# Performance work log

Measured on AMD Instinct MI355X. Metric: run time of the kernel, lower is better.

Reference implementation:

```python
import jax, jax.numpy as jnp
import numpy as np

T = 40           # rollout steps
ATT_TEMP = 5.0   # Arbiter attention temperature
ACT_CLIP = 3.5


def setup_inputs() -> dict:
    key = jax.random.key(0)
    ks = jax.random.split(key, 6)
    B, D = 262144, 128
    # states: vel >= 0, dx > 0 (dx is a divisor)
    unscaled_s = jax.random.uniform(ks[0], (B, T, 7), dtype=jnp.float32)
    unscaled_s = unscaled_s.at[:, :, 0].set(unscaled_s[:, :, 0] * 20.0 + 5.0)   # vel
    unscaled_s = unscaled_s.at[:, :, 2].set(unscaled_s[:, :, 2] * 4.0 - 2.0)    # dv (leader)
    unscaled_s = unscaled_s.at[:, :, 3].set(unscaled_s[:, :, 3] * 50.0 + 10.0)  # dx (leader)
    unscaled_s = unscaled_s.at[:, :, 5].set(unscaled_s[:, :, 5] * 4.0 - 2.0)    # dv (merger)
    unscaled_s = unscaled_s.at[:, :, 6].set(unscaled_s[:, :, 6] * 50.0 + 10.0)  # dx (merger)
    # idm params: all strictly positive (sqrt + division)
    p = jax.random.uniform(ks[1], (B, 5), dtype=jnp.float32)
    idm_param = jnp.stack([
        p[:, 0] * 10.0 + 20.0,  # desired_v
        p[:, 1] * 1.0 + 0.5,    # desired_tgap
        p[:, 2] * 3.0 + 1.0,    # min_jamx
        p[:, 3] * 2.0 + 0.5,    # max_act
        p[:, 4] * 2.0 + 0.5,    # min_act
    ], axis=1)
    decoder_output = jax.random.normal(ks[2], (B, D), dtype=jnp.float32)
    W1 = jax.random.normal(ks[3], (D, 100), dtype=jnp.float32) * 0.05
    b1 = jnp.zeros((100,), dtype=jnp.float32)
    W2 = jax.random.normal(ks[4], (100, T), dtype=jnp.float32) * 0.05
    b2 = jnp.zeros((T,), dtype=jnp.float32)
    return {"unscaled_s": unscaled_s, "idm_param": idm_param,
            "decoder_output": decoder_output, "W1": W1, "b1": b1, "W2": W2, "b2": b2}


def _idm_driver(vel, dv, dx, idm_param):
    # vel/dv/dx: [B, T, 1]; idm_param: [B, 5]
    p = idm_param[:, None, :]  # [B, 1, 5]
    desired_v, desired_tgap, min_jamx, max_act, min_act = (
        p[..., 0:1], p[..., 1:2], p[..., 2:3], p[..., 3:4], p[..., 4:5])
    desired_gap = min_jamx + desired_tgap * vel + vel * dv / (2.0 * jnp.sqrt(max_act * min_act))
    act = max_act * (1.0 - (vel / desired_v) ** 4 - (desired_gap / dx) ** 2)
    return jnp.clip(act, -ACT_CLIP, ACT_CLIP)


def reference(unscaled_s, idm_param, decoder_output, W1, b1, W2, b2):
    B = unscaled_s.shape[0]
    # The 40-step loop has no cross-step dependency -> fully vectorized over T.
    s = unscaled_s[:, :T, :]                 # [B, T, 7]
    vel = s[:, :, 0:1]
    fl_seq = _idm_driver(vel, s[:, :, 2:3], s[:, :, 3:4], idm_param)  # [B, T, 1]
    fm_seq = _idm_driver(vel, s[:, :, 5:6], s[:, :, 6:7], idm_param)  # [B, T, 1]
    # Arbiter: two dense layers + temperature sigmoid
    h = decoder_output @ W1 + b1
    logits = h @ W2 + b2                      # [B, T]
    att_scores = jax.nn.sigmoid(ATT_TEMP * logits).reshape(B, T, 1)
    act_seq = att_scores * fl_seq + (1.0 - att_scores) * fm_seq
    return act_seq, att_scores
```

## Files before the change

kernel.cpp:

```cpp
#include <hip/hip_runtime.h>


#define TT 40
#define DD 128
#define ACT_CLIP 3.5f
#define ATT_TEMP 5.0f

typedef short short8 __attribute__((ext_vector_type(8)));
typedef float f32x4 __attribute__((ext_vector_type(4)));

__device__ __forceinline__ unsigned int bf16_rne(float v) {
    unsigned int u = __float_as_uint(v);
    return (u + 0x7FFFu + ((u >> 16) & 1u)) >> 16;
}

__global__ __launch_bounds__(256) void precompute_pack(
    const float* __restrict__ W1, const float* __restrict__ b1,
    const float* __restrict__ W2, const float* __restrict__ b2,
    unsigned int* __restrict__ wpack,
    float* __restrict__ bcp)
{
    int idx = blockIdx.x * 256 + threadIdx.x;
    if (idx < 1536) {
        int l   = idx & 63;
        int rec = idx >> 6;
        int h   = rec & 1;
        int sn  = rec >> 1;
        int n   = sn % 3, s = sn / 3;
        int col = n * 16 + (l & 15);
        int k0  = s * 32 + (l >> 4) * 8;
        unsigned short hv[8];
#pragma unroll
        for (int j = 0; j < 8; ++j) {
            float v = 0.0f;
            if (col < TT) {
                int k = k0 + j;
                for (int m = 0; m < 100; ++m)
                    v = fmaf(W1[k * 100 + m], W2[m * TT + col], v);
            }
            unsigned int hi = bf16_rne(v);
            float hif = __uint_as_float(hi << 16);
            unsigned int lo = bf16_rne(v - hif);
            hv[j] = (unsigned short)(h == 0 ? hi : lo);
        }
        uint4 o;
        o.x = hv[0] | ((unsigned)hv[1] << 16);
        o.y = hv[2] | ((unsigned)hv[3] << 16);
        o.z = hv[4] | ((unsigned)hv[5] << 16);
        o.w = hv[6] | ((unsigned)hv[7] << 16);
        reinterpret_cast<uint4*>(wpack)[idx] = o;
    } else if (idx < 1536 + 48) {
        int t = idx - 1536;
        float v = 0.0f;
        if (t < TT) {
            v = b2[t];
            for (int m = 0; m < 100; ++m)
                v = fmaf(b1[m], W2[m * TT + t], v);
        }
        bcp[t] = v;
    }
}

__global__ __launch_bounds__(256, 4) void matvec_att(
    const float* __restrict__ x,
    const unsigned int* __restrict__ wpack,
    const float* __restrict__ bcp,
    float* __restrict__ attout)
{
    __shared__ unsigned int swp[6144];
    __shared__ float sbc[48];
    __shared__ float satt[64 * TT];

    int tid = threadIdx.x;
    {
        const uint4* src = reinterpret_cast<const uint4*>(wpack);
        uint4* dst = reinterpret_cast<uint4*>(swp);
#pragma unroll
        for (int i = 0; i < 6; ++i) dst[tid + 256 * i] = src[tid + 256 * i];
        if (tid < 48) sbc[tid] = bcp[tid];
    }
    __syncthreads();

    int wave = tid >> 6, lane = tid & 63;
    int l15 = lane & 15, lk = lane >> 4;
    size_t blk = blockIdx.x;
    size_t row0 = blk * 64 + wave * 16 + l15;
    const float* xr = x + row0 * DD;

    float4 xv[8];
#pragma unroll
    for (int s = 0; s < 4; ++s) {
        xv[2 * s]     = *reinterpret_cast<const float4*>(xr + s * 32 + lk * 8);
        xv[2 * s + 1] = *reinterpret_cast<const float4*>(xr + s * 32 + lk * 8 + 4);
    }

    f32x4 acc[3] = {f32x4{0,0,0,0}, f32x4{0,0,0,0}, f32x4{0,0,0,0}};

#pragma unroll
    for (int s = 0; s < 4; ++s) {
        float fs[8] = {xv[2*s].x, xv[2*s].y, xv[2*s].z, xv[2*s].w,
                       xv[2*s+1].x, xv[2*s+1].y, xv[2*s+1].z, xv[2*s+1].w};
        union { unsigned int u[4]; short8 v; } ah, al;
#pragma unroll
        for (int p = 0; p < 4; ++p) {
            unsigned int u0 = __float_as_uint(fs[2*p]);
            unsigned int u1 = __float_as_uint(fs[2*p+1]);
            ah.u[p] = (u0 >> 16) | (u1 & 0xFFFF0000u);
            float r0 = fs[2*p]   - __uint_as_float(u0 & 0xFFFF0000u);
            float r1 = fs[2*p+1] - __uint_as_float(u1 & 0xFFFF0000u);
            al.u[p] = (__float_as_uint(r0) >> 16) |
                      (__float_as_uint(r1) & 0xFFFF0000u);
        }
#pragma unroll
        for (int n = 0; n < 3; ++n) {
            int base = (s * 3 + n) * 512;
            short8 bh = *reinterpret_cast<const short8*>(&swp[base + lane * 4]);
            short8 bl = *reinterpret_cast<const short8*>(&swp[base + 256 + lane * 4]);
            acc[n] = __builtin_amdgcn_mfma_f32_16x16x32_bf16(ah.v, bh, acc[n], 0, 0, 0);
            acc[n] = __builtin_amdgcn_mfma_f32_16x16x32_bf16(al.v, bh, acc[n], 0, 0, 0);
            acc[n] = __builtin_amdgcn_mfma_f32_16x16x32_bf16(ah.v, bl, acc[n], 0, 0, 0);
        }
    }

#pragma unroll
    for (int n = 0; n < 3; ++n) {
        int col = n * 16 + l15;
        if (col < TT) {
            float bias = sbc[col];
#pragma unroll
            for (int r = 0; r < 4; ++r) {
                int rowl = wave * 16 + lk * 4 + r;
                float L = acc[n][r] + bias;
                satt[rowl * TT + col] =
                    __builtin_amdgcn_rcpf(1.0f + __expf(-ATT_TEMP * L));
            }
        }
    }
    __syncthreads();

    float4* dst = reinterpret_cast<float4*>(attout + blk * 64 * TT);
    const float4* s4 = reinterpret_cast<const float4*>(satt);
    dst[tid]       = s4[tid];
    dst[tid + 256] = s4[tid + 256];
    if (tid < 128) dst[tid + 512] = s4[tid + 512];
}

__global__ __launch_bounds__(320) void epilogue_k(
    const float* __restrict__ us, const float* __restrict__ prm,
    const float* __restrict__ attg,
    float* __restrict__ act)
{
    __shared__ float sus[320 * 31];

    int tid = threadIdx.x;
    size_t blk = blockIdx.x;

    f32x4 a4 = reinterpret_cast<const f32x4*>(attg)[blk * 320u + tid];

    const f32x4* su = reinterpret_cast<const f32x4*>(us) + blk * 2240u;
#pragma unroll
    for (int i = 0; i < 7; ++i) {
        unsigned f = (unsigned)tid + 320u * i;
        f32x4 v = su[f];
        unsigned item = f / 7u;
        unsigned slot = f - item * 7u;
        float* w = &sus[item * 31u + slot * 4u];
        w[0] = v.x; w[1] = v.y; w[2] = v.z; w[3] = v.w;
    }

    unsigned int row_g = (unsigned)(blk * 320u + tid) / 10u;
    const float* pr = prm + (size_t)row_g * 5u;
    float desired_v    = pr[0];
    float desired_tgap = pr[1];
    float min_jamx     = pr[2];
    float max_act      = pr[3];
    float min_act      = pr[4];

    __syncthreads();

    float inv_dv = __builtin_amdgcn_rcpf(desired_v);
    float coef   = 0.5f / sqrtf(max_act * min_act);

    const float* fp = &sus[(unsigned)tid * 31u];
    float ares[4];
#pragma unroll
    for (int tt = 0; tt < 4; ++tt) {
        float vel = fp[tt * 7 + 0];
        float dvl = fp[tt * 7 + 2], dxl = fp[tt * 7 + 3];
        float dvm = fp[tt * 7 + 5], dxm = fp[tt * 7 + 6];

        float r  = vel * inv_dv;
        float r2 = r * r;
        float common = 1.0f - r2 * r2;
        float base = fmaf(desired_tgap, vel, min_jamx);
        float gl = fmaf(vel * dvl, coef, base);
        float gm = fmaf(vel * dvm, coef, base);
        float ql = gl * __builtin_amdgcn_rcpf(dxl);
        float qm = gm * __builtin_amdgcn_rcpf(dxm);
        float al = max_act * (common - ql * ql);
        float am = max_act * (common - qm * qm);
        al = fminf(fmaxf(al, -ACT_CLIP), ACT_CLIP);
        am = fminf(fmaxf(am, -ACT_CLIP), ACT_CLIP);
        float a = (tt == 0) ? a4.x : (tt == 1) ? a4.y : (tt == 2) ? a4.z : a4.w;
        ares[tt] = fmaf(a, al - am, am);
    }
    f32x4 res = {ares[0], ares[1], ares[2], ares[3]};
    reinterpret_cast<f32x4*>(act)[blk * 320u + tid] = res;
}

extern "C" void kernel_launch(void* const* d_in, const int* in_sizes, int n_in,
                              void* d_out, int out_size, void* d_ws, size_t ws_size,
                              hipStream_t stream) {
    const float* us  = (const float*)d_in[0];
    const float* prm = (const float*)d_in[1];
    const float* x   = (const float*)d_in[2];
    const float* W1  = (const float*)d_in[3];
    const float* b1  = (const float*)d_in[4];
    const float* W2  = (const float*)d_in[5];
    const float* b2  = (const float*)d_in[6];
    float* out = (float*)d_out;

    int B = in_sizes[1] / 5;

    unsigned int* wpack = (unsigned int*)d_ws;
    float* bcp = (float*)((char*)d_ws + 24576);

    float* attout = out + (size_t)B * TT;

    hipLaunchKernelGGL(precompute_pack, dim3(7), dim3(256), 0, stream,
                       W1, b1, W2, b2, wpack, bcp);
    hipLaunchKernelGGL(matvec_att, dim3(B / 64), dim3(256), 0, stream,
                       x, wpack, bcp, attout);
    hipLaunchKernelGGL(epilogue_k, dim3(B / 32), dim3(320), 0, stream,
                       us, prm, attout, out);
}
```

Before: 131.3 us.

## Fuse attention matvec and IDM epilogue into warp-specialized pipelined kernel

Merges the MFMA attention kernel and the IDM epilogue into a single kernel. Two waves compute attention logits for 32-row chunks into double-buffered shared memory while five other waves stream unscaled_s into LDS and compute the blended action, with each block handling four strided chunks. This removes the global round-trip of the attention scores between kernels and the per-block reload of packed weights, which are now kept in registers. In exchange, only two MFMA waves per block produce attention, many __syncthreads couple the two roles, and the large per-thread register footprint may limit occupancy.

Result: slower. 148.5 us (+13.1%).

```diff
diff --git a/kernel.cpp b/kernel.cpp
--- a/kernel.cpp
+++ b/kernel.cpp
@@ -3,6 +3,7 @@
 
 #define TT 40
 #define DD 128
+#define CPB 4
 #define ACT_CLIP 3.5f
 #define ATT_TEMP 5.0f
 
@@ -61,151 +62,178 @@
     }
 }
 
-__global__ __launch_bounds__(256, 4) void matvec_att(
+__global__ __launch_bounds__(448) void fused_pipe(
     const float* __restrict__ x,
     const unsigned int* __restrict__ wpack,
     const float* __restrict__ bcp,
-    float* __restrict__ attout)
-{
-    __shared__ unsigned int swp[6144];
-    __shared__ float sbc[48];
-    __shared__ float satt[64 * TT];
-
-    int tid = threadIdx.x;
-    {
-        const uint4* src = reinterpret_cast<const uint4*>(wpack);
-        uint4* dst = reinterpret_cast<uint4*>(swp);
-#pragma unroll
-        for (int i = 0; i < 6; ++i) dst[tid + 256 * i] = src[tid + 256 * i];
-        if (tid < 48) sbc[tid] = bcp[tid];
-    }
-    __syncthreads();
-
-    int wave = tid >> 6, lane = tid & 63;
-    int l15 = lane & 15, lk = lane >> 4;
-    size_t blk = blockIdx.x;
-    size_t row0 = blk * 64 + wave * 16 + l15;
-    const float* xr = x + row0 * DD;
-
-    float4 xv[8];
-#pragma unroll
-    for (int s = 0; s < 4; ++s) {
-        xv[2 * s]     = *reinterpret_cast<const float4*>(xr + s * 32 + lk * 8);
-        xv[2 * s + 1] = *reinterpret_cast<const float4*>(xr + s * 32 + lk * 8 + 4);
-    }
-
-    f32x4 acc[3] = {f32x4{0,0,0,0}, f32x4{0,0,0,0}, f32x4{0,0,0,0}};
-
-#pragma unroll
-    for (int s = 0; s < 4; ++s) {
-        float fs[8] = {xv[2*s].x, xv[2*s].y, xv[2*s].z, xv[2*s].w,
-                       xv[2*s+1].x, xv[2*s+1].y, xv[2*s+1].z, xv[2*s+1].w};
-        union { unsigned int u[4]; short8 v; } ah, al;
-#pragma unroll
-        for (int p = 0; p < 4; ++p) {
-            unsigned int u0 = __float_as_uint(fs[2*p]);
-            unsigned int u1 = __float_as_uint(fs[2*p+1]);
-            ah.u[p] = (u0 >> 16) | (u1 & 0xFFFF0000u);
-            float r0 = fs[2*p]   - __uint_as_float(u0 & 0xFFFF0000u);
-            float r1 = fs[2*p+1] - __uint_as_float(u1 & 0xFFFF0000u);
-            al.u[p] = (__float_as_uint(r0) >> 16) |
-                      (__float_as_uint(r1) & 0xFFFF0000u);
-        }
-#pragma unroll
-        for (int n = 0; n < 3; ++n) {
-            int base = (s * 3 + n) * 512;
-            short8 bh = *reinterpret_cast<const short8*>(&swp[base + lane * 4]);
-            short8 bl = *reinterpret_cast<const short8*>(&swp[base + 256 + lane * 4]);
-            acc[n] = __builtin_amdgcn_mfma_f32_16x16x32_bf16(ah.v, bh, acc[n], 0, 0, 0);
-            acc[n] = __builtin_amdgcn_mfma_f32_16x16x32_bf16(al.v, bh, acc[n], 0, 0, 0);
-            acc[n] = __builtin_amdgcn_mfma_f32_16x16x32_bf16(ah.v, bl, acc[n], 0, 0, 0);
-        }
-    }
-
-#pragma unroll
-    for (int n = 0; n < 3; ++n) {
-        int col = n * 16 + l15;
-        if (col < TT) {
-            float bias = sbc[col];
-#pragma unroll
-            for (int r = 0; r < 4; ++r) {
-                int rowl = wave * 16 + lk * 4 + r;
-                float L = acc[n][r] + bias;
-                satt[rowl * TT + col] =
-                    __builtin_amdgcn_rcpf(1.0f + __expf(-ATT_TEMP * L));
-            }
-        }
-    }
-    __syncthreads();
-
-    float4* dst = reinterpret_cast<float4*>(attout + blk * 64 * TT);
-    const float4* s4 = reinterpret_cast<const float4*>(satt);
-    dst[tid]       = s4[tid];
-    dst[tid + 256] = s4[tid + 256];
-    if (tid < 128) dst[tid + 512] = s4[tid + 512];
-}
-
-__global__ __launch_bounds__(320) void epilogue_k(
-    const float* __restrict__ us, const float* __restrict__ prm,
-    const float* __restrict__ attg,
-    float* __restrict__ act)
+    const float* __restrict__ us,
+    const float* __restrict__ prm,
+    float* __restrict__ act,
+    float* __restrict__ attout,
+    int nb)
 {
     __shared__ float sus[320 * 31];
-
-    int tid = threadIdx.x;
-    size_t blk = blockIdx.x;
-
-    f32x4 a4 = reinterpret_cast<const f32x4*>(attg)[blk * 320u + tid];
-
-    const f32x4* su = reinterpret_cast<const f32x4*>(us) + blk * 2240u;
-#pragma unroll
-    for (int i = 0; i < 7; ++i) {
-        unsigned f = (unsigned)tid + 320u * i;
-        f32x4 v = su[f];
-        unsigned item = f / 7u;
-        unsigned slot = f - item * 7u;
-        float* w = &sus[item * 31u + slot * 4u];
-        w[0] = v.x; w[1] = v.y; w[2] = v.z; w[3] = v.w;
+    __shared__ float satt[2][32 * TT];
+
+    const int tid = threadIdx.x;
+    const unsigned blk = blockIdx.x;
+
+    if (tid < 128) {
+        const int wave = tid >> 6, lane = tid & 63;
+        const int l15 = lane & 15, lk = lane >> 4;
+
+        short8 wbh[12], wbl[12];
+#pragma unroll
+        for (int sn = 0; sn < 12; ++sn) {
+            int base = sn * 512;
+            wbh[sn] = *reinterpret_cast<const short8*>(&wpack[base + lane * 4]);
+            wbl[sn] = *reinterpret_cast<const short8*>(&wpack[base + 256 + lane * 4]);
+        }
+        float bias[3];
+#pragma unroll
+        for (int n = 0; n < 3; ++n) {
+            int col = n * 16 + l15;
+            bias[n] = (col < TT) ? bcp[col] : 0.0f;
+        }
+
+        float4 xv[8];
+        auto mm_load = [&](unsigned cid) {
+            const float* xr = x + ((size_t)cid * 32 + wave * 16 + l15) * DD;
+#pragma unroll
+            for (int s = 0; s < 4; ++s) {
+                xv[2*s]   = *reinterpret_cast<const float4*>(xr + s * 32 + lk * 8);
+                xv[2*s+1] = *reinterpret_cast<const float4*>(xr + s * 32 + lk * 8 + 4);
+            }
+        };
+        auto mm_compute = [&](int buf) {
+            f32x4 acc[3] = {f32x4{0,0,0,0}, f32x4{0,0,0,0}, f32x4{0,0,0,0}};
+#pragma unroll
+            for (int s = 0; s < 4; ++s) {
+                float fs[8] = {xv[2*s].x, xv[2*s].y, xv[2*s].z, xv[2*s].w,
+                               xv[2*s+1].x, xv[2*s+1].y, xv[2*s+1].z, xv[2*s+1].w};
+                union { unsigned int u[4]; short8 v; } ah, al;
+#pragma unroll
+                for (int p = 0; p < 4; ++p) {
+                    unsigned int u0 = __float_as_uint(fs[2*p]);
+                    unsigned int u1 = __float_as_uint(fs[2*p+1]);
+                    ah.u[p] = (u0 >> 16) | (u1 & 0xFFFF0000u);
+                    float r0 = fs[2*p]   - __uint_as_float(u0 & 0xFFFF0000u);
+                    float r1 = fs[2*p+1] - __uint_as_float(u1 & 0xFFFF0000u);
+                    al.u[p] = (__float_as_uint(r0) >> 16) |
+                              (__float_as_uint(r1) & 0xFFFF0000u);
+                }
+#pragma unroll
+                for (int n = 0; n < 3; ++n) {
+                    acc[n] = __builtin_amdgcn_mfma_f32_16x16x32_bf16(ah.v, wbh[s*3+n], acc[n], 0, 0, 0);
+                    acc[n] = __builtin_amdgcn_mfma_f32_16x16x32_bf16(al.v, wbh[s*3+n], acc[n], 0, 0, 0);
+                    acc[n] = __builtin_amdgcn_mfma_f32_16x16x32_bf16(ah.v, wbl[s*3+n], acc[n], 0, 0, 0);
+                }
+            }
+#pragma unroll
+            for (int n = 0; n < 3; ++n) {
+                int col = n * 16 + l15;
+                if (col < TT) {
+#pragma unroll
+                    for (int r = 0; r < 4; ++r) {
+                        int rowl = wave * 16 + lk * 4 + r;
+                        float L = acc[n][r] + bias[n];
+                        satt[buf][rowl * TT + col] =
+                            __builtin_amdgcn_rcpf(1.0f + __expf(-ATT_TEMP * L));
+                    }
+                }
+            }
+        };
+
+        mm_load(blk);
+        mm_compute(0);
+#pragma unroll
+        for (int c = 0; c < CPB; ++c) {
+            __syncthreads();
+            if (c + 1 < CPB) mm_load(blk + (unsigned)nb * (c + 1));
+            __syncthreads();
+            if (c + 1 < CPB) mm_compute((c + 1) & 1);
+        }
+    } else {
+        const int et = tid - 128;
+
+        f32x4 rvA[7], rvB[7];
+        auto ep_issue = [&](unsigned cid, f32x4* rv) {
+            const f32x4* su = reinterpret_cast<const f32x4*>(us) + (size_t)cid * 2240u;
+#pragma unroll
+            for (int i = 0; i < 7; ++i) rv[i] = su[et + 320 * i];
+        };
+        auto ep_write = [&](const f32x4* rv) {
+#pragma unroll
+            for (int i = 0; i < 7; ++i) {
+                unsigned f = (unsigned)et + 320u * i;
+                unsigned item = f / 7u;
+                unsigned slot = f - item * 7u;
+                float* w = &sus[item * 31u + slot * 4u];
+                w[0] = rv[i].x; w[1] = rv[i].y; w[2] = rv[i].z; w[3] = rv[i].w;
+            }
+        };
+        auto ep_consume = [&](unsigned cid, int buf) {
+            unsigned row_g = cid * 32u + (unsigned)et / 10u;
+            const float* pr = prm + (size_t)row_g * 5u;
+            float desired_v    = pr[0];
+            float desired_tgap = pr[1];
+            float min_jamx     = pr[2];
+            float max_act      = pr[3];
+            float min_act      = pr[4];
+            float inv_dv = __builtin_amdgcn_rcpf(desired_v);
+            float coef   = 0.5f / sqrtf(max_act * min_act);
+
+            f32x4 a4 = reinterpret_cast<const f32x4*>(&satt[buf][0])[et];
+            const float* fp = &sus[(unsigned)et * 31u];
+            float ares[4];
+#pragma unroll
+            for (int tt = 0; tt < 4; ++tt) {
+                float vel = fp[tt * 7 + 0];
+                float dvl = fp[tt * 7 + 2], dxl = fp[tt * 7 + 3];
+                float dvm = fp[tt * 7 + 5], dxm = fp[tt * 7 + 6];
+
+                float r  = vel * inv_dv;
+                float r2 = r * r;
+                float common = 1.0f - r2 * r2;
+                float base = fmaf(desired_tgap, vel, min_jamx);
+                float gl = fmaf(vel * dvl, coef, base);
+                float gm = fmaf(vel * dvm, coef, base);
+                float ql = gl * __builtin_amdgcn_rcpf(dxl);
+                float qm = gm * __builtin_amdgcn_rcpf(dxm);
+                float al = max_act * (common - ql * ql);
+                float am = max_act * (common - qm * qm);
+                al = fminf(fmaxf(al, -ACT_CLIP), ACT_CLIP);
+                am = fminf(fmaxf(am, -ACT_CLIP), ACT_CLIP);
+                float a = (tt==0) ? a4.x : (tt==1) ? a4.y : (tt==2) ? a4.z : a4.w;
+                ares[tt] = fmaf(a, al - am, am);
+            }
+            f32x4 res = {ares[0], ares[1], ares[2], ares[3]};
+            reinterpret_cast<f32x4*>(act)[(size_t)cid * 320u + et] = res;
+            reinterpret_cast<f32x4*>(attout)[(size_t)cid * 320u + et] = a4;
+        };
+
+        unsigned nbu = (unsigned)nb;
+        ep_issue(blk, rvA);
+        __syncthreads();
+        ep_write(rvA);
+        ep_issue(blk + nbu, rvB);
+        __syncthreads();
+        ep_consume(blk, 0);
+        __syncthreads();
+        ep_write(rvB);
+        ep_issue(blk + 2u * nbu, rvA);
+        __syncthreads();
+        ep_consume(blk + nbu, 1);
+        __syncthreads();
+        ep_write(rvA);
+        ep_issue(blk + 3u * nbu, rvB);
+        __syncthreads();
+        ep_consume(blk + 2u * nbu, 0);
+        __syncthreads();
+        ep_write(rvB);
+        __syncthreads();
+        ep_consume(blk + 3u * nbu, 1);
     }
-
-    unsigned int row_g = (unsigned)(blk * 320u + tid) / 10u;
-    const float* pr = prm + (size_t)row_g * 5u;
-    float desired_v    = pr[0];
-    float desired_tgap = pr[1];
-    float min_jamx     = pr[2];
-    float max_act      = pr[3];
-    float min_act      = pr[4];
-
-    __syncthreads();
-
-    float inv_dv = __builtin_amdgcn_rcpf(desired_v);
-    float coef   = 0.5f / sqrtf(max_act * min_act);
-
-    const float* fp = &sus[(unsigned)tid * 31u];
-    float ares[4];
-#pragma unroll
-    for (int tt = 0; tt < 4; ++tt) {
-        float vel = fp[tt * 7 + 0];
-        float dvl = fp[tt * 7 + 2], dxl = fp[tt * 7 + 3];
-        float dvm = fp[tt * 7 + 5], dxm = fp[tt * 7 + 6];
-
-        float r  = vel * inv_dv;
-        float r2 = r * r;
-        float common = 1.0f - r2 * r2;
-        float base = fmaf(desired_tgap, vel, min_jamx);
-        float gl = fmaf(vel * dvl, coef, base);
-        float gm = fmaf(vel * dvm, coef, base);
-        float ql = gl * __builtin_amdgcn_rcpf(dxl);
-        float qm = gm * __builtin_amdgcn_rcpf(dxm);
-        float al = max_act * (common - ql * ql);
-        float am = max_act * (common - qm * qm);
-        al = fminf(fmaxf(al, -ACT_CLIP), ACT_CLIP);
-        am = fminf(fmaxf(am, -ACT_CLIP), ACT_CLIP);
-        float a = (tt == 0) ? a4.x : (tt == 1) ? a4.y : (tt == 2) ? a4.z : a4.w;
-        ares[tt] = fmaf(a, al - am, am);
-    }
-    f32x4 res = {ares[0], ares[1], ares[2], ares[3]};
-    reinterpret_cast<f32x4*>(act)[blk * 320u + tid] = res;
 }
 
 extern "C" void kernel_launch(void* const* d_in, const int* in_sizes, int n_in,
@@ -221,6 +249,8 @@
     float* out = (float*)d_out;
 
     int B = in_sizes[1] / 5;
+    int chunks = B / 32;
+    int nb = chunks / CPB;
 
     unsigned int* wpack = (unsigned int*)d_ws;
     float* bcp = (float*)((char*)d_ws + 24576);
@@ -229,8 +259,6 @@
 
     hipLaunchKernelGGL(precompute_pack, dim3(7), dim3(256), 0, stream,
                        W1, b1, W2, b2, wpack, bcp);
-    hipLaunchKernelGGL(matvec_att, dim3(B / 64), dim3(256), 0, stream,
-                       x, wpack, bcp, attout);
-    hipLaunchKernelGGL(epilogue_k, dim3(B / 32), dim3(320), 0, stream,
-                       us, prm, attout, out);
-}
+    hipLaunchKernelGGL(fused_pipe, dim3(nb), dim3(448), 0, stream,
+                       x, wpack, bcp, us, prm, out, attout, nb);
+}
```
